# Kernel optimization log

Hardware: AMD Instinct MI355X
Metric: run time of the kernel (lower is better)

The kernel has to match this reference:

```python
import jax, jax.numpy as jnp
import numpy as np

B, S, D, H = 2, 2048, 2048, 16
HD = D // H  # head_dim = 128


def setup_inputs() -> dict:
    key = jax.random.key(0)
    ks = jax.random.split(key, 5)
    scale = 1.0 / np.sqrt(D)
    return {
        "x": jax.random.normal(ks[0], (B, S, D), dtype=jnp.float32),
        "Wq": jax.random.normal(ks[1], (D, D), dtype=jnp.float32) * scale,
        "Wk": jax.random.normal(ks[2], (D, D), dtype=jnp.float32) * scale,
        "Wv": jax.random.normal(ks[3], (D, D), dtype=jnp.float32) * scale,
        "Wo": jax.random.normal(ks[4], (D, D), dtype=jnp.float32) * scale,
    }


def reference(x, Wq, Wk, Wv, Wo):
    # torch Linear: y = x @ W.T (weight is [out, in], no bias)
    b, s, d = x.shape
    def split_heads(t):
        return t.reshape(b, s, H, HD).transpose(0, 2, 1, 3)  # [B,H,S,HD]
    q = split_heads(x @ Wq.T)
    k = split_heads(x @ Wk.T)
    v = split_heads(x @ Wv.T)
    scores = jnp.einsum("bhqd,bhkd->bhqk", q, k) / jnp.sqrt(jnp.float32(HD))
    attn = jax.nn.softmax(scores, axis=-1)
    out = jnp.einsum("bhqk,bhkd->bhqd", attn, v)  # [B,H,S,HD]
    out = out.transpose(0, 2, 1, 3).reshape(b, s, d)
    return out @ Wo.T
```

## Files before the change

### kernel.cpp

```cpp
#include <hip/hip_runtime.h>
#include <stdint.h>

typedef unsigned short u16t;
typedef short bf16x8 __attribute__((ext_vector_type(8)));
typedef float f32x4 __attribute__((ext_vector_type(4)));

#define B_ 2
#define S_ 2048
#define D_ 2048
#define H_ 16
#define HD_ 128

#define MFMA16(a,b,c) __builtin_amdgcn_mfma_f32_16x16x32_bf16((a),(b),(c),0,0,0)

typedef const __attribute__((address_space(1))) void* gptr_t;
typedef __attribute__((address_space(3))) void* lptr_t;
#define GLL16(src, dst) __builtin_amdgcn_global_load_lds((gptr_t)(src), (lptr_t)(dst), 16, 0, 0)

__device__ __forceinline__ u16t f2bf(float f) {
  uint32_t u = __builtin_bit_cast(uint32_t, f);
  u = (u + 0x7fffu + ((u >> 16) & 1u)) >> 16;
  return (u16t)u;
}

__global__ void cvt_kernel(const float* __restrict__ in, u16t* __restrict__ out, int n8) {
  int i = blockIdx.x * blockDim.x + threadIdx.x;
  if (i >= n8) return;
  const float4* p = (const float4*)in + (size_t)i * 2;
  float4 a = p[0], b = p[1];
  union { u16t u[8]; uint4 v; } pk;
  pk.u[0]=f2bf(a.x); pk.u[1]=f2bf(a.y); pk.u[2]=f2bf(a.z); pk.u[3]=f2bf(a.w);
  pk.u[4]=f2bf(b.x); pk.u[5]=f2bf(b.y); pk.u[6]=f2bf(b.z); pk.u[7]=f2bf(b.w);
  *(uint4*)(out + (size_t)i * 8) = pk.v;
}

__global__ void wcvt_kernel(const float* __restrict__ w0, const float* __restrict__ w1,
                            const float* __restrict__ w2, const float* __restrict__ w3,
                            u16t* o0, u16t* o1, u16t* o2, u16t* o3) {
  int blk = blockIdx.x;
  int wsel = blk >> 11;
  const float* in = (wsel == 0) ? w0 : (wsel == 1) ? w1 : (wsel == 2) ? w2 : w3;
  u16t* out = (wsel == 0) ? o0 : (wsel == 1) ? o1 : (wsel == 2) ? o2 : o3;
  int i = (blk & 2047) * 256 + threadIdx.x;
  const float4* p = (const float4*)in + (size_t)i * 2;
  float4 a = p[0], b = p[1];
  union { u16t u[8]; uint4 v; } pk;
  pk.u[0]=f2bf(a.x); pk.u[1]=f2bf(a.y); pk.u[2]=f2bf(a.z); pk.u[3]=f2bf(a.w);
  pk.u[4]=f2bf(b.x); pk.u[5]=f2bf(b.y); pk.u[6]=f2bf(b.z); pk.u[7]=f2bf(b.w);
  *(uint4*)(out + (size_t)i * 8) = pk.v;
}

template<int OUT_BF16>
__global__ __launch_bounds__(256, 2) void gemm_bt(const u16t* __restrict__ A,
                                                  const u16t* __restrict__ Bw,
                                                  void* __restrict__ Cout,
                                                  int Mtiles, int Ntiles, int K,
                                                  float alpha) {
  __shared__ __attribute__((aligned(16))) u16t Al[2][128*32];
  __shared__ __attribute__((aligned(16))) u16t Bl[2][128*32];
  int nwg = Mtiles * Ntiles;
  int bid = blockIdx.x;
  int wg  = ((bid & 7) * (nwg >> 3)) + (bid >> 3);
  int mt = wg / Ntiles, nt = wg % Ntiles;
  int t = threadIdx.x, lane = t & 63, w = t >> 6;
  int wm = w >> 1, wn = w & 1;
  int c = lane & 15, g = lane >> 4;

  const u16t* Ag = A  + (size_t)mt * 128 * K;
  const u16t* Bg = Bw + (size_t)nt * 128 * K;

  auto stage = [&](int buf, int kt) {
    int k0 = kt * 32;
    #pragma unroll
    for (int i = 0; i < 2; i++) {
      int r = (i*256 + t) >> 2;
      int x = t & 3;
      int xs = x ^ ((r >> 1) & 3);
      GLL16(Ag + (size_t)r * K + k0 + xs*8, &Al[buf][(i*256 + (t & ~63)) * 8]);
    }
    #pragma unroll
    for (int i = 0; i < 2; i++) {
      int r = (i*256 + t) >> 2;
      int x = t & 3;
      int xs = x ^ ((r >> 1) & 3);
      GLL16(Bg + (size_t)r * K + k0 + xs*8, &Bl[buf][(i*256 + (t & ~63)) * 8]);
    }
  };

  f32x4 acc[4][4];
  #pragma unroll
  for (int mi = 0; mi < 4; mi++)
    #pragma unroll
    for (int ni = 0; ni < 4; ni++) acc[mi][ni] = (f32x4){0.f,0.f,0.f,0.f};

  int nk = K >> 5;
  stage(0, 0);
  int cur = 0;
  int slot = (g ^ ((c >> 1) & 3)) * 8;
  for (int kt = 0; kt < nk; ++kt) {
    __syncthreads();
    if (kt + 1 < nk) stage(cur ^ 1, kt + 1);
    bf16x8 af[4], bfg[4];
    #pragma unroll
    for (int mi = 0; mi < 4; mi++) {
      int r = wm*64 + mi*16 + c;
      af[mi] = *(const bf16x8*)&Al[cur][r*32 + slot];
    }
    #pragma unroll
    for (int ni = 0; ni < 4; ni++) {
      int r = wn*64 + ni*16 + c;
      bfg[ni] = *(const bf16x8*)&Bl[cur][r*32 + slot];
    }
    #pragma unroll
    for (int mi = 0; mi < 4; mi++)
      #pragma unroll
      for (int ni = 0; ni < 4; ni++)
        acc[mi][ni] = MFMA16(af[mi], bfg[ni], acc[mi][ni]);
    cur ^= 1;
  }

  size_t Ng = (size_t)Ntiles * 128;
  int m0 = mt*128 + wm*64 + 4*g;
  int n0 = nt*128 + wn*64 + c;
  if (OUT_BF16) {
    u16t* C = (u16t*)Cout;
    #pragma unroll
    for (int mi = 0; mi < 4; mi++)
      #pragma unroll
      for (int ni = 0; ni < 4; ni++)
        #pragma unroll
        for (int r = 0; r < 4; r++)
          C[(size_t)(m0 + 16*mi + r) * Ng + n0 + 16*ni] = f2bf(acc[mi][ni][r] * alpha);
  } else {
    float* C = (float*)Cout;
    #pragma unroll
    for (int mi = 0; mi < 4; mi++)
      #pragma unroll
      for (int ni = 0; ni < 4; ni++)
        #pragma unroll
        for (int r = 0; r < 4; r++)
          C[(size_t)(m0 + 16*mi + r) * Ng + n0 + 16*ni] = acc[mi][ni][r] * alpha;
  }
}

__global__ void vtrans_kernel(const u16t* __restrict__ V, u16t* __restrict__ Vt) {
  __shared__ __attribute__((aligned(16))) u16t T[64][72];
  int bid = blockIdx.x;
  int dt = bid & 1;
  int st = (bid >> 1) & 31;
  int head = bid >> 6;
  int b = head >> 4, h = head & 15;
  int t = threadIdx.x;
  #pragma unroll
  for (int p = 0; p < 2; p++) {
    int sr = p*32 + (t >> 3), x = t & 7;
    uint4 v = *(const uint4*)&V[(size_t)(b*S_ + st*64 + sr)*D_ + h*HD_ + dt*64 + x*8];
    *(uint4*)&T[sr][x*8] = v;
  }
  __syncthreads();
  #pragma unroll
  for (int p = 0; p < 2; p++) {
    int dr = p*32 + (t >> 3), x = t & 7;
    union { u16t u[8]; uint4 v; } pk;
    #pragma unroll
    for (int j = 0; j < 8; j++) pk.u[j] = T[x*8 + j][dr];
    *(uint4*)&Vt[(size_t)(head*HD_ + dt*64 + dr)*S_ + st*64 + x*8] = pk.v;
  }
}

__global__ __launch_bounds__(256, 2) void attn_kernel(const u16t* __restrict__ Q,
                                                      const u16t* __restrict__ Kg,
                                                      const u16t* __restrict__ Vt,
                                                      u16t* __restrict__ O) {
  __shared__ __attribute__((aligned(16))) u16t Kl[2][64*128];
  __shared__ __attribute__((aligned(16))) u16t Vl[2][128*64];
  __shared__ __attribute__((aligned(16))) u16t Pl[4][32*64];
  int bid = blockIdx.x;
  int qt = bid & 15, head = bid >> 4;
  int b = head >> 4, h = head & 15;
  int t = threadIdx.x, lane = t & 63, w = t >> 6;
  int c = lane & 15, g = lane >> 4;
  int q0 = qt*128 + w*32;

  bf16x8 qf[2][4];
  #pragma unroll
  for (int mi = 0; mi < 2; mi++)
    #pragma unroll
    for (int ks = 0; ks < 4; ks++)
      qf[mi][ks] = *(const bf16x8*)&Q[(size_t)(b*S_ + q0 + c + 16*mi)*D_ + h*HD_ + 8*g + 32*ks];

  f32x4 oacc[8][2];
  #pragma unroll
  for (int mf = 0; mf < 8; mf++) { oacc[mf][0] = (f32x4){0,0,0,0}; oacc[mf][1] = (f32x4){0,0,0,0}; }
  f32x4 lacc[2];
  lacc[0] = (f32x4){0,0,0,0}; lacc[1] = (f32x4){0,0,0,0};
  bf16x8 ones;
  #pragma unroll
  for (int j = 0; j < 8; j++) ones[j] = (short)0x3F80;

  auto stageK = [&](int buf, int kt) {
    int s0 = kt*64;
    #pragma unroll
    for (int i = 0; i < 4; i++) {
      int row = (i*256 + t) >> 4;
      int xs = (t & 15) ^ (row & 15);
      GLL16(&Kg[(size_t)(b*S_ + s0 + row)*D_ + h*HD_ + xs*8], &Kl[buf][(i*256 + (t & ~63))*8]);
    }
  };
  auto stageV = [&](int buf, int kt) {
    int s0 = kt*64;
    #pragma unroll
    for (int i = 0; i < 4; i++) {
      int d = (i*256 + t) >> 3;
      int xs = (t & 7) ^ (d & 7);
      GLL16(&Vt[(size_t)(head*HD_ + d)*S_ + s0 + xs*8], &Vl[buf][(i*256 + (t & ~63))*8]);
    }
  };

  stageK(0, 0); stageV(0, 0);
  int cur = 0;
  for (int kt = 0; kt < 32; ++kt) {
    __syncthreads();
    if (kt + 1 < 32) { stageK(cur ^ 1, kt + 1); stageV(cur ^ 1, kt + 1); }

    f32x4 sacc[2][4];
    #pragma unroll
    for (int mi = 0; mi < 2; mi++)
      #pragma unroll
      for (int nf = 0; nf < 4; nf++) sacc[mi][nf] = (f32x4){0,0,0,0};
    #pragma unroll
    for (int ks = 0; ks < 4; ks++) {
      #pragma unroll
      for (int nf = 0; nf < 4; nf++) {
        bf16x8 kf = *(const bf16x8*)&Kl[cur][(c + 16*nf)*128 + (((g + 4*ks) ^ c) & 15)*8];
        sacc[0][nf] = MFMA16(qf[0][ks], kf, sacc[0][nf]);
        sacc[1][nf] = MFMA16(qf[1][ks], kf, sacc[1][nf]);
      }
    }

    #pragma unroll
    for (int mi = 0; mi < 2; mi++)
      #pragma unroll
      for (int nf = 0; nf < 4; nf++)
        #pragma unroll
        for (int reg = 0; reg < 4; reg++) {
          float p = __expf(sacc[mi][nf][reg]);
          int r = 16*mi + 4*g + reg;
          int col = c + 16*nf;
          Pl[w][r*64 + ((((col >> 3) ^ (r & 7)) & 7) << 3) + (col & 7)] = f2bf(p);
        }

    #pragma unroll
    for (int ks = 0; ks < 2; ks++) {
      int ps = ((g + 4*ks) ^ (c & 7)) & 7;
      bf16x8 pf0 = *(const bf16x8*)&Pl[w][(c      )*64 + ps*8];
      bf16x8 pf1 = *(const bf16x8*)&Pl[w][(c + 16 )*64 + ps*8];
      lacc[0] = MFMA16(ones, pf0, lacc[0]);
      lacc[1] = MFMA16(ones, pf1, lacc[1]);
      #pragma unroll
      for (int mf = 0; mf < 8; mf++) {
        bf16x8 vf = *(const bf16x8*)&Vl[cur][(c + 16*mf)*64 + ps*8];
        oacc[mf][0] = MFMA16(vf, pf0, oacc[mf][0]);
        oacc[mf][1] = MFMA16(vf, pf1, oacc[mf][1]);
      }
    }
    cur ^= 1;
  }

  float li0 = 1.f / lacc[0][0];
  float li1 = 1.f / lacc[1][0];
  #pragma unroll
  for (int mf = 0; mf < 8; mf++) {
    #pragma unroll
    for (int nf = 0; nf < 2; nf++) {
      float liv = nf ? li1 : li0;
      union { u16t u[4]; uint2 v; } pk;
      #pragma unroll
      for (int r = 0; r < 4; r++) pk.u[r] = f2bf(oacc[mf][nf][r] * liv);
      int qrow = q0 + c + 16*nf;
      int d0 = 16*mf + 4*g;
      *(uint2*)&O[(size_t)(b*S_ + qrow)*D_ + h*HD_ + d0] = pk.v;
    }
  }
}

extern "C" void kernel_launch(void* const* d_in, const int* in_sizes, int n_in,
                              void* d_out, int out_size, void* d_ws, size_t ws_size,
                              hipStream_t stream) {
  const float* x  = (const float*)d_in[0];
  const float* Wq = (const float*)d_in[1];
  const float* Wk = (const float*)d_in[2];
  const float* Wv = (const float*)d_in[3];
  const float* Wo = (const float*)d_in[4];

  const size_t M1 = 1024*1024;
  u16t* ws  = (u16t*)d_ws;
  u16t* xb  = ws;
  u16t* Wqb = xb  + 8*M1;
  u16t* Wkb = Wqb + 4*M1;
  u16t* Wvb = Wkb + 4*M1;
  u16t* Wob = Wvb + 4*M1;
  u16t* Qb  = Wob + 4*M1;
  u16t* Vb  = (u16t*)d_out;
  u16t* Kb  = (u16t*)d_out + 8*M1;
  u16t* Vtb = xb;
  u16t* AOb = Wqb;

  const float scl = 0.08838834764831845f;

  cvt_kernel<<<4096, 256, 0, stream>>>(x, xb, 1048576);
  wcvt_kernel<<<8192, 256, 0, stream>>>(Wq, Wk, Wv, Wo, Wqb, Wkb, Wvb, Wob);

  gemm_bt<1><<<512, 256, 0, stream>>>(xb, Wqb, Qb, 32, 16, 2048, scl);
  gemm_bt<1><<<512, 256, 0, stream>>>(xb, Wkb, Kb, 32, 16, 2048, 1.0f);
  gemm_bt<1><<<512, 256, 0, stream>>>(xb, Wvb, Vb, 32, 16, 2048, 1.0f);

  vtrans_kernel<<<2048, 256, 0, stream>>>(Vb, Vtb);

  attn_kernel<<<512, 256, 0, stream>>>(Qb, Kb, Vtb, AOb);

  gemm_bt<0><<<512, 256, 0, stream>>>(AOb, Wob, d_out, 32, 16, 2048, 1.0f);
}
```

Before: 415.8 us.

## Replace GEMM with 256x256 tiled 512-thread kernel and fuse QKV projections

Replaces the 128x128-tile GEMM with a 256x256-tile, 512-thread kernel. It uses K-steps of 64, a two-stage LDS prefetch, and global-to-LDS loads interleaved between MFMA quadrants with raised wave priority. The three Q/K/V projections become a single launch that picks the weight and output pointer per N-tile, which removes two launches and shares one schedule across the three. The bigger tiles cut global traffic per FLOP, but they use about 128KB of LDS per block. The output projection now launches only 128 blocks, which may leave many CUs idle.

```diff
diff --git a/kernel.cpp b/kernel.cpp
--- a/kernel.cpp
+++ b/kernel.cpp
@@ -51,95 +51,129 @@
 }
 
 template<int OUT_BF16>
-__global__ __launch_bounds__(256, 2) void gemm_bt(const u16t* __restrict__ A,
-                                                  const u16t* __restrict__ Bw,
-                                                  void* __restrict__ Cout,
-                                                  int Mtiles, int Ntiles, int K,
-                                                  float alpha) {
-  __shared__ __attribute__((aligned(16))) u16t Al[2][128*32];
-  __shared__ __attribute__((aligned(16))) u16t Bl[2][128*32];
+__global__ __launch_bounds__(512, 2) void gemm256(const u16t* __restrict__ A,
+                                                  const u16t* __restrict__ Bw0,
+                                                  const u16t* __restrict__ Bw1,
+                                                  const u16t* __restrict__ Bw2,
+                                                  void* __restrict__ C0,
+                                                  void* __restrict__ C1,
+                                                  void* __restrict__ C2,
+                                                  int Mtiles, int Ntiles, int tpw,
+                                                  int K, float a0, float a1, float a2) {
+  __shared__ __attribute__((aligned(16))) u16t Al[2][2][128*64];
+  __shared__ __attribute__((aligned(16))) u16t Bl[2][2][128*64];
   int nwg = Mtiles * Ntiles;
   int bid = blockIdx.x;
   int wg  = ((bid & 7) * (nwg >> 3)) + (bid >> 3);
   int mt = wg / Ntiles, nt = wg % Ntiles;
+  int wsel = nt / tpw;
+  const u16t* Bw = (wsel == 0) ? Bw0 : (wsel == 1) ? Bw1 : Bw2;
+  const u16t* Ag = A  + (size_t)mt * 256 * K;
+  const u16t* Bg = Bw + (size_t)(nt - wsel*tpw) * 256 * K;
+
   int t = threadIdx.x, lane = t & 63, w = t >> 6;
-  int wm = w >> 1, wn = w & 1;
+  int wm = w >> 2, wn = w & 3;
   int c = lane & 15, g = lane >> 4;
 
-  const u16t* Ag = A  + (size_t)mt * 128 * K;
-  const u16t* Bg = Bw + (size_t)nt * 128 * K;
-
-  auto stage = [&](int buf, int kt) {
-    int k0 = kt * 32;
-    #pragma unroll
-    for (int i = 0; i < 2; i++) {
-      int r = (i*256 + t) >> 2;
-      int x = t & 3;
-      int xs = x ^ ((r >> 1) & 3);
-      GLL16(Ag + (size_t)r * K + k0 + xs*8, &Al[buf][(i*256 + (t & ~63)) * 8]);
-    }
-    #pragma unroll
-    for (int i = 0; i < 2; i++) {
-      int r = (i*256 + t) >> 2;
-      int x = t & 3;
-      int xs = x ^ ((r >> 1) & 3);
-      GLL16(Bg + (size_t)r * K + k0 + xs*8, &Bl[buf][(i*256 + (t & ~63)) * 8]);
-    }
-  };
-
-  f32x4 acc[4][4];
-  #pragma unroll
-  for (int mi = 0; mi < 4; mi++)
-    #pragma unroll
-    for (int ni = 0; ni < 4; ni++) acc[mi][ni] = (f32x4){0.f,0.f,0.f,0.f};
-
-  int nk = K >> 5;
-  stage(0, 0);
-  int cur = 0;
-  int slot = (g ^ ((c >> 1) & 3)) * 8;
+  auto stageA = [&](int buf, int hf, int kt) {
+    #pragma unroll
+    for (int j = 0; j < 2; j++) {
+      int s = j*512 + t;
+      int row = s >> 3;
+      int ks = (s & 7) ^ (row & 7);
+      GLL16(Ag + (size_t)(hf*128 + row) * K + kt*64 + ks*8,
+            &Al[buf][hf][(j*512 + (t & ~63)) * 8]);
+    }
+  };
+  auto stageB = [&](int buf, int hf, int kt) {
+    #pragma unroll
+    for (int j = 0; j < 2; j++) {
+      int s = j*512 + t;
+      int row = s >> 3;
+      int ks = (s & 7) ^ (row & 7);
+      GLL16(Bg + (size_t)(hf*128 + row) * K + kt*64 + ks*8,
+            &Bl[buf][hf][(j*512 + (t & ~63)) * 8]);
+    }
+  };
+
+  f32x4 acc[8][4];
+  #pragma unroll
+  for (int mf = 0; mf < 8; mf++)
+    #pragma unroll
+    for (int nf = 0; nf < 4; nf++) acc[mf][nf] = (f32x4){0.f,0.f,0.f,0.f};
+
+  int nk = K >> 6;
+  stageA(0,0,0); stageA(0,1,0); stageB(0,0,0); stageB(0,1,0);
+  stageA(1,0,1); stageA(1,1,1); stageB(1,0,1); stageB(1,1,1);
+
+  int sAo[2];
+  #pragma unroll
+  for (int ks = 0; ks < 2; ks++) sAo[ks] = (((ks*4 + g) ^ (c & 7)) << 3);
+  int arow = c * 64;
+  int brow = ((wn & 1) * 64 + c) * 64;
+
+  bf16x8 Af[8][2], Bf[4][2];
+  auto quad = [&](int MF0, int NF0) {
+    __builtin_amdgcn_s_setprio(1);
+    #pragma unroll
+    for (int mq = 0; mq < 4; mq++)
+      #pragma unroll
+      for (int nq = 0; nq < 2; nq++)
+        #pragma unroll
+        for (int ks = 0; ks < 2; ks++)
+          acc[MF0+mq][NF0+nq] = MFMA16(Af[MF0+mq][ks], Bf[NF0+nq][ks], acc[MF0+mq][NF0+nq]);
+    __builtin_amdgcn_s_setprio(0);
+  };
+
   for (int kt = 0; kt < nk; ++kt) {
-    __syncthreads();
-    if (kt + 1 < nk) stage(cur ^ 1, kt + 1);
-    bf16x8 af[4], bfg[4];
-    #pragma unroll
-    for (int mi = 0; mi < 4; mi++) {
-      int r = wm*64 + mi*16 + c;
-      af[mi] = *(const bf16x8*)&Al[cur][r*32 + slot];
-    }
-    #pragma unroll
-    for (int ni = 0; ni < 4; ni++) {
-      int r = wn*64 + ni*16 + c;
-      bfg[ni] = *(const bf16x8*)&Bl[cur][r*32 + slot];
-    }
-    #pragma unroll
-    for (int mi = 0; mi < 4; mi++)
-      #pragma unroll
-      for (int ni = 0; ni < 4; ni++)
-        acc[mi][ni] = MFMA16(af[mi], bfg[ni], acc[mi][ni]);
-    cur ^= 1;
-  }
-
-  size_t Ng = (size_t)Ntiles * 128;
-  int m0 = mt*128 + wm*64 + 4*g;
-  int n0 = nt*128 + wn*64 + c;
+    int p = kt & 1;
+    if (kt < nk - 1) asm volatile("s_waitcnt vmcnt(8)" ::: "memory");
+    else             asm volatile("s_waitcnt vmcnt(0)" ::: "memory");
+    __builtin_amdgcn_s_barrier();
+    #pragma unroll
+    for (int mf = 0; mf < 8; mf++)
+      #pragma unroll
+      for (int ks = 0; ks < 2; ks++)
+        Af[mf][ks] = *(const bf16x8*)&Al[p][wm][mf*1024 + arow + sAo[ks]];
+    #pragma unroll
+    for (int nf = 0; nf < 4; nf++)
+      #pragma unroll
+      for (int ks = 0; ks < 2; ks++)
+        Bf[nf][ks] = *(const bf16x8*)&Bl[p][wn >> 1][nf*1024 + brow + sAo[ks]];
+    quad(0, 0);
+    asm volatile("s_waitcnt lgkmcnt(0)" ::: "memory");
+    __builtin_amdgcn_s_barrier();
+    if (kt + 2 < nk) { stageA(p, 0, kt + 2); stageA(p, 1, kt + 2); }
+    quad(0, 2);
+    __builtin_amdgcn_s_barrier();
+    if (kt + 2 < nk) { stageB(p, 0, kt + 2); stageB(p, 1, kt + 2); }
+    quad(4, 0);
+    __builtin_amdgcn_s_barrier();
+    quad(4, 2);
+  }
+
+  float alpha = (wsel == 0) ? a0 : (wsel == 1) ? a1 : a2;
+  void* Cv = (wsel == 0) ? C0 : (wsel == 1) ? C1 : C2;
+  int m0 = mt*256 + wm*128 + 4*g;
+  int n0 = (nt - wsel*tpw)*256 + wn*64 + c;
   if (OUT_BF16) {
-    u16t* C = (u16t*)Cout;
-    #pragma unroll
-    for (int mi = 0; mi < 4; mi++)
-      #pragma unroll
-      for (int ni = 0; ni < 4; ni++)
+    u16t* C = (u16t*)Cv;
+    #pragma unroll
+    for (int mf = 0; mf < 8; mf++)
+      #pragma unroll
+      for (int nf = 0; nf < 4; nf++)
         #pragma unroll
         for (int r = 0; r < 4; r++)
-          C[(size_t)(m0 + 16*mi + r) * Ng + n0 + 16*ni] = f2bf(acc[mi][ni][r] * alpha);
+          C[(size_t)(m0 + 16*mf + r) * D_ + n0 + 16*nf] = f2bf(acc[mf][nf][r] * alpha);
   } else {
-    float* C = (float*)Cout;
-    #pragma unroll
-    for (int mi = 0; mi < 4; mi++)
-      #pragma unroll
-      for (int ni = 0; ni < 4; ni++)
+    float* C = (float*)Cv;
+    #pragma unroll
+    for (int mf = 0; mf < 8; mf++)
+      #pragma unroll
+      for (int nf = 0; nf < 4; nf++)
         #pragma unroll
         for (int r = 0; r < 4; r++)
-          C[(size_t)(m0 + 16*mi + r) * Ng + n0 + 16*ni] = acc[mi][ni][r] * alpha;
+          C[(size_t)(m0 + 16*mf + r) * D_ + n0 + 16*nf] = acc[mf][nf][r] * alpha;
   }
 }
 
@@ -311,13 +345,13 @@
   cvt_kernel<<<4096, 256, 0, stream>>>(x, xb, 1048576);
   wcvt_kernel<<<8192, 256, 0, stream>>>(Wq, Wk, Wv, Wo, Wqb, Wkb, Wvb, Wob);
 
-  gemm_bt<1><<<512, 256, 0, stream>>>(xb, Wqb, Qb, 32, 16, 2048, scl);
-  gemm_bt<1><<<512, 256, 0, stream>>>(xb, Wkb, Kb, 32, 16, 2048, 1.0f);
-  gemm_bt<1><<<512, 256, 0, stream>>>(xb, Wvb, Vb, 32, 16, 2048, 1.0f);
+  gemm256<1><<<384, 512, 0, stream>>>(xb, Wqb, Wkb, Wvb, Qb, Kb, Vb,
+                                      16, 24, 8, 2048, scl, 1.0f, 1.0f);
 
   vtrans_kernel<<<2048, 256, 0, stream>>>(Vb, Vtb);
 
   attn_kernel<<<512, 256, 0, stream>>>(Qb, Kb, Vtb, AOb);
 
-  gemm_bt<0><<<512, 256, 0, stream>>>(AOb, Wob, d_out, 32, 16, 2048, 1.0f);
-}
+  gemm256<0><<<128, 512, 0, stream>>>(AOb, Wob, Wob, Wob, d_out, d_out, d_out,
+                                      16, 8, 8, 2048, 1.0f, 1.0f, 1.0f);
+}
```

New measurement: 393.4 us. 1.06x faster.
